# Kernel tuning notes

Measured on AMD Instinct MI355X. Metric: run time of the kernel, lower is better.

## Reference

```python
import jax, jax.numpy as jnp
import numpy as np
import math

T, B, C, H, W = 1, 64, 512, 8, 8
E, NH, MEM, FF = 512, 8, 32, 2048
HD = E // NH            # 64 per-head channels
TOT = HD * H * W        # 4096 = flattened per-head dim (channels x spatial)


def conv2d(x, w, b):
    # NCHW conv with 'same' padding, matching torch.nn.Conv2d(padding='same')
    y = jax.lax.conv_general_dilated(x, w, (1, 1), 'SAME',
                                     dimension_numbers=('NCHW', 'OIHW', 'NCHW'))
    return y + b[None, :, None, None]


def layernorm(x, w, b, eps=1e-5):
    # LayerNorm over (C,H,W) with elementwise affine, matching nn.LayerNorm((C,H,W))
    m = jnp.mean(x, axis=(1, 2, 3), keepdims=True)
    v = jnp.var(x, axis=(1, 2, 3), keepdims=True)
    return (x - m) * jax.lax.rsqrt(v + eps) * w[None] + b[None]


def setup_inputs() -> dict:
    key = jax.random.key(0)
    ks = jax.random.split(key, 16)
    s = 0.02
    inp = {
        'input': jax.random.normal(ks[0], (T, B, C, H, W), jnp.float32),
        'attn_mask': jax.random.randint(ks[1], (B * NH, T, MEM), 0, 2) == 1,
        'concat_k': jax.random.normal(ks[2], (B, MEM, NH, TOT), jnp.float32),
        'concat_v': jax.random.normal(ks[3], (B, MEM, NH, TOT), jnp.float32),
        'proj_w': jax.random.normal(ks[4], (3 * E, C, 3, 3), jnp.float32) * s,
        'proj_b': jnp.zeros((3 * E,), jnp.float32),
        'out_w': jax.random.normal(ks[5], (E, E, 3, 3), jnp.float32) * s,
        'out_b': jnp.zeros((E,), jnp.float32),
        'lin1_w': jax.random.normal(ks[6], (FF, E, 3, 3), jnp.float32) * s,
        'lin1_b': jnp.zeros((FF,), jnp.float32),
        'lin2_w': jax.random.normal(ks[7], (E, FF, 3, 3), jnp.float32) * s,
        'lin2_b': jnp.zeros((E,), jnp.float32),
        'n1_w': jnp.ones((E, H, W), jnp.float32),
        'n1_b': jnp.zeros((E, H, W), jnp.float32),
        'n2_w': jnp.ones((E, H, W), jnp.float32),
        'n2_b': jnp.zeros((E, H, W), jnp.float32),
        'pos_w': jax.random.normal(ks[8], (MEM, H * W * E), jnp.float32) * s,
        'pos_b': jax.random.uniform(ks[9], (MEM, NH), jnp.float32, -0.1, 0.1),
    }
    return inp


def reference(input, attn_mask, concat_k, concat_v, proj_w, proj_b, out_w, out_b,
              lin1_w, lin1_b, lin2_w, lin2_b, n1_w, n1_b, n2_w, n2_b, pos_w, pos_b):
    x = input.reshape(T * B, C, H, W)
    kqv = conv2d(x, proj_w, proj_b)                      # [B, 3E, H, W]
    k0, q0, v0 = kqv[:, :E], kqv[:, E:2 * E], kqv[:, 2 * E:]

    def split_heads(t):  # [T*B,E,H,W] -> [B*NH, T, TOT]
        return t.reshape(T, B * NH, HD, H, W).transpose(1, 0, 2, 3, 4).reshape(B * NH, T, TOT)

    k, q, v = split_heads(k0), split_heads(q0), split_heads(v0)
    q = q / math.sqrt(TOT)

    def mem_pre(c):  # [B,MEM,NH,TOT] -> [B*NH, MEM-1, TOT]
        return c[:, 1:].transpose(1, 0, 2, 3).reshape(MEM - 1, B * NH, TOT).transpose(1, 0, 2)

    k = jnp.concatenate([mem_pre(concat_k), k], axis=1)  # [B*NH, MEM, TOT]
    v = jnp.concatenate([mem_pre(concat_v), v], axis=1)

    # learned relative-position bias on keys and logits
    pw = jnp.broadcast_to(pos_w[:, None, :], (MEM, B, NH * TOT)).reshape(MEM, B * NH, TOT).transpose(1, 0, 2)
    pb = jnp.broadcast_to(pos_b[:, None, :], (MEM, B, NH)).reshape(MEM, B * NH).transpose(1, 0)
    k = k + pw

    mask = jnp.where(attn_mask, -jnp.inf, 0.0).astype(q.dtype)
    mask = mask.at[:, :, -1].set(5.0)                    # current step always attendable (+5 bias)
    logits = mask + jnp.einsum('bqd,bkd->bqk', q, k) + pb[:, None, :]
    w_attn = jax.nn.softmax(logits, axis=-1)             # [B*NH, T, MEM]
    attn = jnp.einsum('bqk,bkd->bqd', w_attn, v)         # [B*NH, T, TOT]
    attn = attn.transpose(1, 0, 2).reshape(B, E, H, W)

    out = conv2d(attn, out_w, out_b)
    ret_k = k.transpose(1, 0, 2).reshape(MEM, B, NH, TOT).transpose(1, 0, 2, 3)
    ret_v = v.transpose(1, 0, 2).reshape(MEM, B, NH, TOT).transpose(1, 0, 2, 3)

    # norm_first=False path
    out = out + x[:, :E]
    out = layernorm(out, n1_w, n1_b)
    ff = conv2d(jax.nn.relu(conv2d(out, lin1_w, lin1_b)), lin2_w, lin2_b)
    out = layernorm(out + ff, n2_w, n2_b)
    return (out[None], ret_k, ret_v)
```

## Files before the change

### kernel.cpp

```cpp
#include <hip/hip_runtime.h>
#include <hip/hip_bf16.h>
#include <stdint.h>

typedef __attribute__((ext_vector_type(8))) short bf16x8;
typedef __attribute__((ext_vector_type(4))) float f32x4;

static __device__ __forceinline__ unsigned short f2bf(float f) {
  union { float f; unsigned int u; } v; v.f = f;
  unsigned int u = v.u;
  return (unsigned short)((u + 0x7FFFu + ((u >> 16) & 1u)) >> 16);
}

static __device__ __forceinline__ void gld16(const void* g, void* l) {
  __builtin_amdgcn_global_load_lds(
      (const __attribute__((address_space(1))) unsigned int*)g,
      (__attribute__((address_space(3))) unsigned int*)l, 16, 0, 0);
}

__global__ __launch_bounds__(256) void k_zero(uint4* __restrict__ p, int n) {
  int i = blockIdx.x * 256 + threadIdx.x;
  if (i < n) p[i] = make_uint4(0u, 0u, 0u, 0u);
}

__global__ __launch_bounds__(256) void k_prep(
    const float* __restrict__ projw, const float* __restrict__ outw,
    const float* __restrict__ l1w, const float* __restrict__ l2w,
    const float* __restrict__ x,
    unsigned short* __restrict__ wbP, unsigned short* __restrict__ wbO,
    unsigned short* __restrict__ wbL1, unsigned short* __restrict__ wbL2,
    unsigned short* __restrict__ xp) {
  __shared__ float l[4608];
  int bid = blockIdx.x, t = threadIdx.x;
  if (bid < 6144) {
    const float* in; unsigned short* out; int o, C, c0;
    if (bid < 1536)      { in = projw; out = wbP;  o = bid;               C = 512;  c0 = 0; }
    else if (bid < 2048) { in = outw;  out = wbO;  o = bid - 1536;        C = 512;  c0 = 0; }
    else if (bid < 4096) { in = l1w;   out = wbL1; o = bid - 2048;        C = 512;  c0 = 0; }
    else                 { in = l2w;   out = wbL2; o = (bid - 4096) >> 2; C = 2048; c0 = ((bid - 4096) & 3) << 9; }
    const float* src = in + ((size_t)o * C + c0) * 9;
    for (int j = t; j < 4608; j += 256) l[j] = src[j];
    __syncthreads();
    unsigned short* dst = out + (size_t)o * 9 * C;
#pragma unroll
    for (int j = 0; j < 18; ++j) {
      int f = t * 18 + j;
      int tap = f >> 9, c = f & 511;
      dst[(size_t)tap * C + c0 + c] = f2bf(l[c * 9 + tap]);
    }
  } else {
    int idx = bid - 6144;
    int b = idx >> 3, c0 = (idx & 7) << 6;
    float (*lt)[65] = (float(*)[65])l;
    int cr = t >> 2, p0 = (t & 3) << 4;
    const float* src = x + ((size_t)b * 512 + c0 + cr) * 64 + p0;
#pragma unroll
    for (int j = 0; j < 4; ++j) {
      float4 v = *(const float4*)(src + j * 4);
      lt[cr][p0 + j * 4 + 0] = v.x; lt[cr][p0 + j * 4 + 1] = v.y;
      lt[cr][p0 + j * 4 + 2] = v.z; lt[cr][p0 + j * 4 + 3] = v.w;
    }
    __syncthreads();
    int pix = t >> 2, cc0 = (t & 3) << 4;
    size_t prow = (size_t)b * 100 + 11 + (pix >> 3) * 10 + (pix & 7);
    unsigned short pk[16];
#pragma unroll
    for (int j = 0; j < 16; ++j) pk[j] = f2bf(lt[cc0 + j][pix]);
    *(uint4*)(xp + prow * 512 + c0 + cc0) = *(const uint4*)pk;
    *(uint4*)(xp + prow * 512 + c0 + cc0 + 8) = *(const uint4*)(pk + 8);
  }
}

__global__ __launch_bounds__(256) void k_x2pad(const float* __restrict__ x,
                                               unsigned short* __restrict__ xp) {
  int b = blockIdx.x >> 3, c0 = (blockIdx.x & 7) << 6;
  int t = threadIdx.x;
  __shared__ float l[64][65];
  int cr = t >> 2, p0 = (t & 3) << 4;
  const float* src = x + ((size_t)b * 512 + c0 + cr) * 64 + p0;
#pragma unroll
  for (int j = 0; j < 4; ++j) {
    float4 v = *(const float4*)(src + j * 4);
    l[cr][p0 + j * 4 + 0] = v.x; l[cr][p0 + j * 4 + 1] = v.y;
    l[cr][p0 + j * 4 + 2] = v.z; l[cr][p0 + j * 4 + 3] = v.w;
  }
  __syncthreads();
  int pix = t >> 2, cc0 = (t & 3) << 4;
  size_t prow = (size_t)b * 100 + 11 + (pix >> 3) * 10 + (pix & 7);
  unsigned short pk[16];
#pragma unroll
  for (int j = 0; j < 16; ++j) pk[j] = f2bf(l[cc0 + j][pix]);
  *(uint4*)(xp + prow * 512 + c0 + cc0) = *(const uint4*)pk;
  *(uint4*)(xp + prow * 512 + c0 + cc0 + 8) = *(const uint4*)(pk + 8);
}

template <int EPI>
__global__ __launch_bounds__(256, 2) void k_gemm9(
    const unsigned short* __restrict__ Wt, int ldK,
    const unsigned short* __restrict__ Xp, int C, int tlog,
    int kiter, const float* __restrict__ bias,
    void* __restrict__ outv, int Cout, size_t zstride) {
  __shared__ unsigned short lds[2][2][8192];
  int t = threadIdx.x, lane = t & 63, wid = t >> 6;

  int gx = gridDim.x;
  int f = blockIdx.x + blockIdx.y * gx;
  int cpx = (gx * gridDim.y) >> 3;
  int fs = (f & 7) * cpx + (f >> 3);
  int bx = fs % gx, by = fs / gx;

  int O0 = bx << 7, M0 = by << 7;
  int kbase = blockIdx.z * kiter;
  int srow = lane >> 3, skg = (lane & 7) << 3;

  int wrow[4], pbv[4];
#pragma unroll
  for (int i = 0; i < 4; ++i) {
    int rl = wid * 8 + i * 32 + srow;
    wrow[i] = O0 + rl;
    int m = M0 + rl, b = m >> 6, pix = m & 63;
    pbv[i] = b * 100 + (pix >> 3) * 10 + (pix & 7);
  }

  f32x4 acc[4][4];
#pragma unroll
  for (int i = 0; i < 4; ++i)
#pragma unroll
    for (int j = 0; j < 4; ++j) acc[i][j] = (f32x4){0.f, 0.f, 0.f, 0.f};

  auto stage = [&](int buf, int kt) {
    int gk = kbase + kt;
    int tap = gk >> tlog;
    int c0 = (gk - (tap << tlog)) << 6;
    int toff = tap + 7 * ((tap * 11) >> 5);
#pragma unroll
    for (int i = 0; i < 4; ++i) {
      gld16(Wt + (size_t)wrow[i] * ldK + (gk << 6) + skg,
            &lds[buf][0][(wid * 8 + i * 32) * 64]);
      gld16(Xp + (size_t)(pbv[i] + toff) * C + c0 + skg,
            &lds[buf][1][(wid * 8 + i * 32) * 64]);
    }
  };

  int wr = wid >> 1, wc = wid & 1;
  int frow = lane & 15, fkb = (lane >> 4) << 3;

  auto compute = [&](int buf) {
    const unsigned short* Wl = &lds[buf][0][0];
    const unsigned short* Xl = &lds[buf][1][0];
#pragma unroll
    for (int kk = 0; kk < 2; ++kk) {
      bf16x8 af[4], bfv[4];
#pragma unroll
      for (int ff = 0; ff < 4; ++ff) {
        af[ff]  = *(const bf16x8*)(Wl + ((wr * 64 + ff * 16 + frow) << 6) + kk * 32 + fkb);
        bfv[ff] = *(const bf16x8*)(Xl + ((wc * 64 + ff * 16 + frow) << 6) + kk * 32 + fkb);
      }
#pragma unroll
      for (int fi = 0; fi < 4; ++fi)
#pragma unroll
        for (int fj = 0; fj < 4; ++fj)
          acc[fi][fj] = __builtin_amdgcn_mfma_f32_16x16x32_bf16(af[fi], bfv[fj], acc[fi][fj], 0, 0, 0);
    }
  };

  stage(0, 0);
  __syncthreads();
  for (int kt = 0; kt < kiter; ++kt) {
    int cur = kt & 1;
    if (kt + 1 < kiter) stage(cur ^ 1, kt + 1);
    compute(cur);
    __syncthreads();
  }

  int ob = O0 + wr * 64, mb = M0 + wc * 64;
  int r0 = (lane >> 4) << 2, cm = lane & 15;
  if (EPI == 4) {
    unsigned short* outp = (unsigned short*)outv;
#pragma unroll
    for (int fi = 0; fi < 4; ++fi) {
      int oo = ob + fi * 16 + r0;
      float4 bv = *(const float4*)(bias + oo);
#pragma unroll
      for (int fj = 0; fj < 4; ++fj) {
        int mm = mb + fj * 16 + cm;
        int bb = mm >> 6, pix = mm & 63;
        size_t prow = (size_t)bb * 100 + 11 + (pix >> 3) * 10 + (pix & 7);
        unsigned short pk[4];
        pk[0] = f2bf(fmaxf(acc[fi][fj][0] + bv.x, 0.f));
        pk[1] = f2bf(fmaxf(acc[fi][fj][1] + bv.y, 0.f));
        pk[2] = f2bf(fmaxf(acc[fi][fj][2] + bv.z, 0.f));
        pk[3] = f2bf(fmaxf(acc[fi][fj][3] + bv.w, 0.f));
        *(ushort4*)(outp + prow * Cout + oo) = *(const ushort4*)pk;
      }
    }
  } else {
    float* out = (float*)outv + (size_t)blockIdx.z * zstride;
#pragma unroll
    for (int fi = 0; fi < 4; ++fi) {
#pragma unroll
      for (int fj = 0; fj < 4; ++fj) {
        int mm = mb + fj * 16 + cm;
        int bb = mm >> 6, pix = mm & 63;
#pragma unroll
        for (int r = 0; r < 4; ++r) {
          int oo = ob + fi * 16 + r0 + r;
          float v = acc[fi][fj][r];
          if (EPI == 0) v += bias[oo];
          out[((size_t)bb * Cout + oo) * 64 + pix] = v;
        }
      }
    }
  }
}

__global__ __launch_bounds__(256) void k_sum2(const float* __restrict__ a,
                                              const float* __restrict__ b,
                                              const float* __restrict__ bias,
                                              float* __restrict__ o) {
  int i = (blockIdx.x * 256 + threadIdx.x) * 4;
  int ch = (i >> 6) % 1536;
  float4 va = *(const float4*)(a + i);
  float4 vb = *(const float4*)(b + i);
  float bs = bias[ch];
  *(float4*)(o + i) = make_float4(va.x + vb.x + bs, va.y + vb.y + bs,
                                  va.z + vb.z + bs, va.w + vb.w + bs);
}

__global__ __launch_bounds__(256) void k_attnK(
    const float* __restrict__ kqv, const float* __restrict__ ck,
    const float* __restrict__ pw, const float* __restrict__ pb,
    float* __restrict__ rk, float* __restrict__ logits) {
  int idx = blockIdx.x;
  int h = idx & 7, m = (idx >> 3) & 31, b = idx >> 8;
  int t = threadIdx.x, lane = t & 63, wid = t >> 6;
  int i0 = t << 4;
  int hd = i0 >> 6, pix = i0 & 63;

  const float* src = (m < 31)
      ? (ck + (((size_t)(b * 32 + m + 1) * 8 + h) << 12) + i0)
      : (kqv + ((size_t)(b * 1536 + h * 64 + hd) << 6) + pix);
  const float* qs = kqv + ((size_t)(b * 1536 + 512 + h * 64 + hd) << 6) + pix;
  const float* pws = pw + ((size_t)m << 15) + (h << 12) + i0;
  float* dst = rk + (((size_t)(b * 32 + m) * 8 + h) << 12) + i0;

  float part = 0.f;
#pragma unroll
  for (int j = 0; j < 4; ++j) {
    float4 a = *(const float4*)(src + j * 4);
    float4 p = *(const float4*)(pws + j * 4);
    float4 q = *(const float4*)(qs + j * 4);
    float4 kk;
    kk.x = a.x + p.x; kk.y = a.y + p.y; kk.z = a.z + p.z; kk.w = a.w + p.w;
    *(float4*)(dst + j * 4) = kk;
    part += 0.015625f * (q.x * kk.x + q.y * kk.y + q.z * kk.z + q.w * kk.w);
  }
#pragma unroll
  for (int s = 32; s; s >>= 1) part += __shfl_xor(part, s);
  __shared__ float red[4];
  if (lane == 0) red[wid] = part;
  __syncthreads();
  if (t == 0)
    logits[((b << 3) + h) * 32 + m] = red[0] + red[1] + red[2] + red[3] + pb[m * 8 + h];
}

__global__ __launch_bounds__(256) void k_attnV(
    const float* __restrict__ kqv, const int* __restrict__ mask,
    const float* __restrict__ cv, const float* __restrict__ logits,
    float* __restrict__ rv, float* __restrict__ attnb) {
  int bh = blockIdx.x, b = bh >> 3, h = bh & 7;
  int t = threadIdx.x;
  int d = (blockIdx.y << 10) + (t << 2);
  int hd = d >> 6, pix = d & 63;

  float lg[32];
#pragma unroll
  for (int j = 0; j < 8; ++j) {
    float4 v = *(const float4*)(logits + bh * 32 + j * 4);
    lg[j * 4 + 0] = v.x; lg[j * 4 + 1] = v.y; lg[j * 4 + 2] = v.z; lg[j * 4 + 3] = v.w;
  }
  float mx = -INFINITY;
#pragma unroll
  for (int m = 0; m < 32; ++m) {
    if (m == 31) lg[m] += 5.0f;
    else if (mask[bh * 32 + m] != 0) lg[m] = -INFINITY;
    mx = fmaxf(mx, lg[m]);
  }
  float sm = 0.f;
#pragma unroll
  for (int m = 0; m < 32; ++m) { lg[m] = __expf(lg[m] - mx); sm += lg[m]; }
  float rs = 1.f / sm;

  float4 acc = make_float4(0.f, 0.f, 0.f, 0.f);
  for (int m = 0; m < 32; ++m) {
    const float* src = (m < 31)
        ? (cv + (((size_t)(b * 32 + m + 1) * 8 + h) << 12) + d)
        : (kqv + ((size_t)(b * 1536 + 1024 + h * 64 + hd) << 6) + pix);
    float4 v = *(const float4*)src;
    *(float4*)(rv + (((size_t)(b * 32 + m) * 8 + h) << 12) + d) = v;
    float wm = lg[m] * rs;
    acc.x += wm * v.x; acc.y += wm * v.y; acc.z += wm * v.z; acc.w += wm * v.w;
  }
  *(float4*)(attnb + ((size_t)(b * 512 + h * 64 + hd) << 6) + pix) = acc;
}

__global__ __launch_bounds__(256) void k_lnstat(
    const float* __restrict__ p, const float* __restrict__ resid,
    const float* __restrict__ bias, float* __restrict__ xbuf,
    float2* __restrict__ stat) {
  int bb = blockIdx.x, seg = blockIdx.y, t = threadIdx.x;
  int lane = t & 63, wid = t >> 6;
  size_t base = (size_t)bb << 15;
  float s = 0.f, sq = 0.f;
#pragma unroll
  for (int j = 0; j < 4; ++j) {
    int i = (seg << 12) + t * 4 + j * 1024;
    float4 v0 = *(const float4*)(p + base + i);
    float4 v1 = *(const float4*)(p + 2097152 + base + i);
    float4 v2 = *(const float4*)(p + 4194304 + base + i);
    float4 v3 = *(const float4*)(p + 6291456 + base + i);
    float4 vr = *(const float4*)(resid + base + i);
    float bs = bias[i >> 6];
    float4 xx;
    xx.x = v0.x + v1.x + v2.x + v3.x + vr.x + bs;
    xx.y = v0.y + v1.y + v2.y + v3.y + vr.y + bs;
    xx.z = v0.z + v1.z + v2.z + v3.z + vr.z + bs;
    xx.w = v0.w + v1.w + v2.w + v3.w + vr.w + bs;
    *(float4*)(xbuf + base + i) = xx;
    s += xx.x + xx.y + xx.z + xx.w;
    sq += xx.x * xx.x + xx.y * xx.y + xx.z * xx.z + xx.w * xx.w;
  }
#pragma unroll
  for (int k = 32; k; k >>= 1) { s += __shfl_xor(s, k); sq += __shfl_xor(sq, k); }
  __shared__ float rsm[4], rqm[4];
  if (lane == 0) { rsm[wid] = s; rqm[wid] = sq; }
  __syncthreads();
  if (t == 0)
    stat[bb * 8 + seg] = make_float2(rsm[0] + rsm[1] + rsm[2] + rsm[3],
                                     rqm[0] + rqm[1] + rqm[2] + rqm[3]);
}

__global__ __launch_bounds__(256) void k_lnapply(
    const float* __restrict__ xbuf, const float2* __restrict__ stat,
    const float* __restrict__ w, const float* __restrict__ beta,
    float* __restrict__ out) {
  int bb = blockIdx.x, seg = blockIdx.y, t = threadIdx.x;
  size_t base = (size_t)bb << 15;
  float s = 0.f, sq = 0.f;
#pragma unroll
  for (int k = 0; k < 8; ++k) {
    float2 st = stat[bb * 8 + k];
    s += st.x; sq += st.y;
  }
  float mean = s * (1.f / 32768.f);
  float var = sq * (1.f / 32768.f) - mean * mean;
  float rinv = rsqrtf(var + 1e-5f);
#pragma unroll
  for (int j = 0; j < 4; ++j) {
    int i = (seg << 12) + t * 4 + j * 1024;
    float4 xx = *(const float4*)(xbuf + base + i);
    float4 vw = *(const float4*)(w + i);
    float4 vt = *(const float4*)(beta + i);
    float4 r;
    r.x = (xx.x - mean) * rinv * vw.x + vt.x;
    r.y = (xx.y - mean) * rinv * vw.y + vt.y;
    r.z = (xx.z - mean) * rinv * vw.z + vt.z;
    r.w = (xx.w - mean) * rinv * vw.w + vt.w;
    *(float4*)(out + base + i) = r;
  }
}

extern "C" void kernel_launch(void* const* d_in, const int* in_sizes, int n_in,
                              void* d_out, int out_size, void* d_ws, size_t ws_size,
                              hipStream_t stream) {
  const float* x     = (const float*)d_in[0];
  const int*   mask  = (const int*)d_in[1];
  const float* ck    = (const float*)d_in[2];
  const float* cv    = (const float*)d_in[3];
  const float* projw = (const float*)d_in[4];
  const float* projb = (const float*)d_in[5];
  const float* outw  = (const float*)d_in[6];
  const float* outb  = (const float*)d_in[7];
  const float* l1w   = (const float*)d_in[8];
  const float* l1b   = (const float*)d_in[9];
  const float* l2w   = (const float*)d_in[10];
  const float* l2b   = (const float*)d_in[11];
  const float* n1w   = (const float*)d_in[12];
  const float* n1b   = (const float*)d_in[13];
  const float* n2w   = (const float*)d_in[14];
  const float* n2b   = (const float*)d_in[15];
  const float* posw  = (const float*)d_in[16];
  const float* posb  = (const float*)d_in[17];

  char* ws = (char*)d_ws;
  unsigned short* wbP   = (unsigned short*)(ws);
  unsigned short* wbO   = (unsigned short*)(ws + 14155776);
  unsigned short* wbL1  = (unsigned short*)(ws + 18874368);
  unsigned short* wbL2  = (unsigned short*)(ws + 37748736);
  unsigned short* xpadI = (unsigned short*)(ws + 56623104);
  unsigned short* apad  = (unsigned short*)(ws + 63176704);
  unsigned short* l1pad = (unsigned short*)(ws + 69730304);
  unsigned short* ffpad = (unsigned short*)(ws + 76283904);
  float* kqvA   = (float*)(ws + 102498304);
  float* kqvB   = (float*)(ws + 127664128);
  float* kqv    = (float*)(ws + 152829952);
  float* logits = (float*)(ws + 177995776);
  float* res    = (float*)(ws + 178061312);
  float* ln1    = (float*)(ws + 211615744);
  float* attnb  = (float*)(ws + 220004352);
  float* xbuf1  = (float*)(ws + 228392960);
  float* xbuf2  = (float*)(ws + 236781568);
  float2* stat1 = (float2*)(ws + 245170176);
  float2* stat2 = (float2*)(ws + 245174272);

  float* out0 = (float*)d_out;
  float* rk = out0 + 2097152;
  float* rv = rk + 67108864;

  k_zero<<<11200, 256, 0, stream>>>((uint4*)(ws + 56623104), 2867200);

  k_prep<<<6656, 256, 0, stream>>>(projw, outw, l1w, l2w, x, wbP, wbO, wbL1, wbL2, xpadI);

  k_gemm9<3><<<dim3(12, 32, 2), 256, 0, stream>>>(wbP, 4608, xpadI, 512, 3, 36, nullptr, kqvA, 1536, 6291456);
  k_sum2<<<6144, 256, 0, stream>>>(kqvA, kqvB, projb, kqv);

  k_attnK<<<16384, 256, 0, stream>>>(kqv, ck, posw, posb, rk, logits);
  k_attnV<<<dim3(512, 4), 256, 0, stream>>>(kqv, mask, cv, logits, rv, attnb);
  k_x2pad<<<512, 256, 0, stream>>>(attnb, apad);

  k_gemm9<3><<<dim3(4, 32, 4), 256, 0, stream>>>(wbO, 4608, apad, 512, 3, 18, nullptr, res, 512, 2097152);
  k_lnstat<<<dim3(64, 8), 256, 0, stream>>>(res, x, outb, xbuf1, stat1);
  k_lnapply<<<dim3(64, 8), 256, 0, stream>>>(xbuf1, stat1, n1w, n1b, ln1);
  k_x2pad<<<512, 256, 0, stream>>>(ln1, l1pad);

  k_gemm9<4><<<dim3(16, 32, 1), 256, 0, stream>>>(wbL1, 4608, l1pad, 512, 3, 72, l1b, ffpad, 2048, 0);

  k_gemm9<3><<<dim3(4, 32, 4), 256, 0, stream>>>(wbL2, 18432, ffpad, 2048, 5, 72, nullptr, res, 512, 2097152);
  k_lnstat<<<dim3(64, 8), 256, 0, stream>>>(res, ln1, l2b, xbuf2, stat2);
  k_lnapply<<<dim3(64, 8), 256, 0, stream>>>(xbuf2, stat2, n2w, n2b, out0);
}
```

Baseline: 750.3 us.

## Fuse split-K sum into attention, zero only pad borders, fuse LN1 with pad

Drops the separate k_sum2 pass: the attention K and V kernels now read both split-K partial buffers and add the projection bias inline. The full-buffer zeroing kernel is replaced by zeroing only the 36 border rows per image inside k_prep. LayerNorm-1 apply and the bf16 padded transpose are merged into one kernel. This saves several launches and full-tensor round trips, but the query partials are now re-read once per memory slot in k_attnK.

New measurement: 769.6 us. +2.6%, slower.

```diff
diff --git a/kernel.cpp b/kernel.cpp
--- a/kernel.cpp
+++ b/kernel.cpp
@@ -15,11 +15,6 @@
   __builtin_amdgcn_global_load_lds(
       (const __attribute__((address_space(1))) unsigned int*)g,
       (__attribute__((address_space(3))) unsigned int*)l, 16, 0, 0);
-}
-
-__global__ __launch_bounds__(256) void k_zero(uint4* __restrict__ p, int n) {
-  int i = blockIdx.x * 256 + threadIdx.x;
-  if (i < n) p[i] = make_uint4(0u, 0u, 0u, 0u);
 }
 
 __global__ __launch_bounds__(256) void k_prep(
@@ -28,15 +23,35 @@
     const float* __restrict__ x,
     unsigned short* __restrict__ wbP, unsigned short* __restrict__ wbO,
     unsigned short* __restrict__ wbL1, unsigned short* __restrict__ wbL2,
-    unsigned short* __restrict__ xp) {
+    unsigned short* __restrict__ xp, unsigned short* __restrict__ apad,
+    unsigned short* __restrict__ l1pad, unsigned short* __restrict__ ffpad) {
+  int bid = blockIdx.x, t = threadIdx.x;
+  if (bid < 9216) {
+    int buf = bid / 2304, rem = bid - buf * 2304;
+    int b = rem / 36, ridx = rem - b * 36;
+    int row;
+    if (ridx < 11) row = ridx;
+    else if (ridx < 25) { int p = ridx - 11; row = 19 + (p >> 1) * 10 + (p & 1); }
+    else row = 89 + (ridx - 25);
+    unsigned short* ptr; int C;
+    switch (buf) {
+      case 0: ptr = xp;    C = 512;  break;
+      case 1: ptr = apad;  C = 512;  break;
+      case 2: ptr = l1pad; C = 512;  break;
+      default: ptr = ffpad; C = 2048; break;
+    }
+    int n16 = C >> 3;
+    if (t < n16) *(uint4*)(ptr + ((size_t)b * 100 + row) * C + t * 8) = make_uint4(0u, 0u, 0u, 0u);
+    return;
+  }
   __shared__ float l[4608];
-  int bid = blockIdx.x, t = threadIdx.x;
-  if (bid < 6144) {
+  int id = bid - 9216;
+  if (id < 6144) {
     const float* in; unsigned short* out; int o, C, c0;
-    if (bid < 1536)      { in = projw; out = wbP;  o = bid;               C = 512;  c0 = 0; }
-    else if (bid < 2048) { in = outw;  out = wbO;  o = bid - 1536;        C = 512;  c0 = 0; }
-    else if (bid < 4096) { in = l1w;   out = wbL1; o = bid - 2048;        C = 512;  c0 = 0; }
-    else                 { in = l2w;   out = wbL2; o = (bid - 4096) >> 2; C = 2048; c0 = ((bid - 4096) & 3) << 9; }
+    if (id < 1536)      { in = projw; out = wbP;  o = id;               C = 512;  c0 = 0; }
+    else if (id < 2048) { in = outw;  out = wbO;  o = id - 1536;        C = 512;  c0 = 0; }
+    else if (id < 4096) { in = l1w;   out = wbL1; o = id - 2048;        C = 512;  c0 = 0; }
+    else                { in = l2w;   out = wbL2; o = (id - 4096) >> 2; C = 2048; c0 = ((id - 4096) & 3) << 9; }
     const float* src = in + ((size_t)o * C + c0) * 9;
     for (int j = t; j < 4608; j += 256) l[j] = src[j];
     __syncthreads();
@@ -48,7 +63,7 @@
       dst[(size_t)tap * C + c0 + c] = f2bf(l[c * 9 + tap]);
     }
   } else {
-    int idx = bid - 6144;
+    int idx = id - 6144;
     int b = idx >> 3, c0 = (idx & 7) << 6;
     float (*lt)[65] = (float(*)[65])l;
     int cr = t >> 2, p0 = (t & 3) << 4;
@@ -213,21 +228,9 @@
   }
 }
 
-__global__ __launch_bounds__(256) void k_sum2(const float* __restrict__ a,
-                                              const float* __restrict__ b,
-                                              const float* __restrict__ bias,
-                                              float* __restrict__ o) {
-  int i = (blockIdx.x * 256 + threadIdx.x) * 4;
-  int ch = (i >> 6) % 1536;
-  float4 va = *(const float4*)(a + i);
-  float4 vb = *(const float4*)(b + i);
-  float bs = bias[ch];
-  *(float4*)(o + i) = make_float4(va.x + vb.x + bs, va.y + vb.y + bs,
-                                  va.z + vb.z + bs, va.w + vb.w + bs);
-}
-
 __global__ __launch_bounds__(256) void k_attnK(
-    const float* __restrict__ kqv, const float* __restrict__ ck,
+    const float* __restrict__ kqvA, const float* __restrict__ kqvB,
+    const float* __restrict__ projb, const float* __restrict__ ck,
     const float* __restrict__ pw, const float* __restrict__ pb,
     float* __restrict__ rk, float* __restrict__ logits) {
   int idx = blockIdx.x;
@@ -236,23 +239,43 @@
   int i0 = t << 4;
   int hd = i0 >> 6, pix = i0 & 63;
 
-  const float* src = (m < 31)
-      ? (ck + (((size_t)(b * 32 + m + 1) * 8 + h) << 12) + i0)
-      : (kqv + ((size_t)(b * 1536 + h * 64 + hd) << 6) + pix);
-  const float* qs = kqv + ((size_t)(b * 1536 + 512 + h * 64 + hd) << 6) + pix;
+  size_t qoff = ((size_t)(b * 1536 + 512 + h * 64 + hd) << 6) + pix;
   const float* pws = pw + ((size_t)m << 15) + (h << 12) + i0;
   float* dst = rk + (((size_t)(b * 32 + m) * 8 + h) << 12) + i0;
+  float bq = projb[512 + h * 64 + hd];
 
   float part = 0.f;
-#pragma unroll
-  for (int j = 0; j < 4; ++j) {
-    float4 a = *(const float4*)(src + j * 4);
-    float4 p = *(const float4*)(pws + j * 4);
-    float4 q = *(const float4*)(qs + j * 4);
-    float4 kk;
-    kk.x = a.x + p.x; kk.y = a.y + p.y; kk.z = a.z + p.z; kk.w = a.w + p.w;
-    *(float4*)(dst + j * 4) = kk;
-    part += 0.015625f * (q.x * kk.x + q.y * kk.y + q.z * kk.z + q.w * kk.w);
+  if (m < 31) {
+    const float* src = ck + (((size_t)(b * 32 + m + 1) * 8 + h) << 12) + i0;
+#pragma unroll
+    for (int j = 0; j < 4; ++j) {
+      float4 a = *(const float4*)(src + j * 4);
+      float4 p = *(const float4*)(pws + j * 4);
+      float4 qa = *(const float4*)(kqvA + qoff + j * 4);
+      float4 qb = *(const float4*)(kqvB + qoff + j * 4);
+      float4 kk;
+      kk.x = a.x + p.x; kk.y = a.y + p.y; kk.z = a.z + p.z; kk.w = a.w + p.w;
+      *(float4*)(dst + j * 4) = kk;
+      part += 0.015625f * ((qa.x + qb.x + bq) * kk.x + (qa.y + qb.y + bq) * kk.y +
+                           (qa.z + qb.z + bq) * kk.z + (qa.w + qb.w + bq) * kk.w);
+    }
+  } else {
+    size_t koff = ((size_t)(b * 1536 + h * 64 + hd) << 6) + pix;
+    float bk = projb[h * 64 + hd];
+#pragma unroll
+    for (int j = 0; j < 4; ++j) {
+      float4 ka = *(const float4*)(kqvA + koff + j * 4);
+      float4 kb = *(const float4*)(kqvB + koff + j * 4);
+      float4 p = *(const float4*)(pws + j * 4);
+      float4 qa = *(const float4*)(kqvA + qoff + j * 4);
+      float4 qb = *(const float4*)(kqvB + qoff + j * 4);
+      float4 kk;
+      kk.x = ka.x + kb.x + bk + p.x; kk.y = ka.y + kb.y + bk + p.y;
+      kk.z = ka.z + kb.z + bk + p.z; kk.w = ka.w + kb.w + bk + p.w;
+      *(float4*)(dst + j * 4) = kk;
+      part += 0.015625f * ((qa.x + qb.x + bq) * kk.x + (qa.y + qb.y + bq) * kk.y +
+                           (qa.z + qb.z + bq) * kk.z + (qa.w + qb.w + bq) * kk.w);
+    }
   }
 #pragma unroll
   for (int s = 32; s; s >>= 1) part += __shfl_xor(part, s);
@@ -264,7 +287,8 @@
 }
 
 __global__ __launch_bounds__(256) void k_attnV(
-    const float* __restrict__ kqv, const int* __restrict__ mask,
+    const float* __restrict__ kqvA, const float* __restrict__ kqvB,
+    const float* __restrict__ projb, const int* __restrict__ mask,
     const float* __restrict__ cv, const float* __restrict__ logits,
     float* __restrict__ rv, float* __restrict__ attnb) {
   int bh = blockIdx.x, b = bh >> 3, h = bh & 7;
@@ -291,13 +315,23 @@
   float rs = 1.f / sm;
 
   float4 acc = make_float4(0.f, 0.f, 0.f, 0.f);
-  for (int m = 0; m < 32; ++m) {
-    const float* src = (m < 31)
-        ? (cv + (((size_t)(b * 32 + m + 1) * 8 + h) << 12) + d)
-        : (kqv + ((size_t)(b * 1536 + 1024 + h * 64 + hd) << 6) + pix);
+  for (int m = 0; m < 31; ++m) {
+    const float* src = cv + (((size_t)(b * 32 + m + 1) * 8 + h) << 12) + d;
     float4 v = *(const float4*)src;
     *(float4*)(rv + (((size_t)(b * 32 + m) * 8 + h) << 12) + d) = v;
     float wm = lg[m] * rs;
+    acc.x += wm * v.x; acc.y += wm * v.y; acc.z += wm * v.z; acc.w += wm * v.w;
+  }
+  {
+    size_t voff = ((size_t)(b * 1536 + 1024 + h * 64 + hd) << 6) + pix;
+    float bv = projb[1024 + h * 64 + hd];
+    float4 va = *(const float4*)(kqvA + voff);
+    float4 vb = *(const float4*)(kqvB + voff);
+    float4 v;
+    v.x = va.x + vb.x + bv; v.y = va.y + vb.y + bv;
+    v.z = va.z + vb.z + bv; v.w = va.w + vb.w + bv;
+    *(float4*)(rv + (((size_t)(b * 32 + 31) * 8 + h) << 12) + d) = v;
+    float wm = lg[31] * rs;
     acc.x += wm * v.x; acc.y += wm * v.y; acc.z += wm * v.z; acc.w += wm * v.w;
   }
   *(float4*)(attnb + ((size_t)(b * 512 + h * 64 + hd) << 6) + pix) = acc;
@@ -367,6 +401,50 @@
     r.w = (xx.w - mean) * rinv * vw.w + vt.w;
     *(float4*)(out + base + i) = r;
   }
+}
+
+__global__ __launch_bounds__(256) void k_lnpad(
+    const float* __restrict__ xbuf, const float2* __restrict__ stat,
+    const float* __restrict__ w, const float* __restrict__ beta,
+    float* __restrict__ ln1, unsigned short* __restrict__ lp) {
+  int b = blockIdx.x >> 3, c0 = (blockIdx.x & 7) << 6;
+  int t = threadIdx.x;
+  float s = 0.f, sq = 0.f;
+#pragma unroll
+  for (int k = 0; k < 8; ++k) {
+    float2 st = stat[b * 8 + k];
+    s += st.x; sq += st.y;
+  }
+  float mean = s * (1.f / 32768.f);
+  float var = sq * (1.f / 32768.f) - mean * mean;
+  float rinv = rsqrtf(var + 1e-5f);
+
+  __shared__ float l[64][65];
+  int cr = t >> 2, p0 = (t & 3) << 4;
+  size_t off = ((size_t)b * 512 + c0 + cr) * 64 + p0;
+  size_t woff = ((size_t)(c0 + cr)) * 64 + p0;
+#pragma unroll
+  for (int j = 0; j < 4; ++j) {
+    float4 xx = *(const float4*)(xbuf + off + j * 4);
+    float4 vw = *(const float4*)(w + woff + j * 4);
+    float4 vt = *(const float4*)(beta + woff + j * 4);
+    float4 r;
+    r.x = (xx.x - mean) * rinv * vw.x + vt.x;
+    r.y = (xx.y - mean) * rinv * vw.y + vt.y;
+    r.z = (xx.z - mean) * rinv * vw.z + vt.z;
+    r.w = (xx.w - mean) * rinv * vw.w + vt.w;
+    *(float4*)(ln1 + off + j * 4) = r;
+    l[cr][p0 + j * 4 + 0] = r.x; l[cr][p0 + j * 4 + 1] = r.y;
+    l[cr][p0 + j * 4 + 2] = r.z; l[cr][p0 + j * 4 + 3] = r.w;
+  }
+  __syncthreads();
+  int pix = t >> 2, cc0 = (t & 3) << 4;
+  size_t prow = (size_t)b * 100 + 11 + (pix >> 3) * 10 + (pix & 7);
+  unsigned short pk[16];
+#pragma unroll
+  for (int j = 0; j < 16; ++j) pk[j] = f2bf(l[cc0 + j][pix]);
+  *(uint4*)(lp + prow * 512 + c0 + cc0) = *(const uint4*)pk;
+  *(uint4*)(lp + prow * 512 + c0 + cc0 + 8) = *(const uint4*)(pk + 8);
 }
 
 extern "C" void kernel_launch(void* const* d_in, const int* in_sizes, int n_in,
@@ -402,7 +480,6 @@
   unsigned short* ffpad = (unsigned short*)(ws + 76283904);
   float* kqvA   = (float*)(ws + 102498304);
   float* kqvB   = (float*)(ws + 127664128);
-  float* kqv    = (float*)(ws + 152829952);
   float* logits = (float*)(ws + 177995776);
   float* res    = (float*)(ws + 178061312);
   float* ln1    = (float*)(ws + 211615744);
@@ -416,21 +493,18 @@
   float* rk = out0 + 2097152;
   float* rv = rk + 67108864;
 
-  k_zero<<<11200, 256, 0, stream>>>((uint4*)(ws + 56623104), 2867200);
-
-  k_prep<<<6656, 256, 0, stream>>>(projw, outw, l1w, l2w, x, wbP, wbO, wbL1, wbL2, xpadI);
+  k_prep<<<15872, 256, 0, stream>>>(projw, outw, l1w, l2w, x,
+                                    wbP, wbO, wbL1, wbL2, xpadI, apad, l1pad, ffpad);
 
   k_gemm9<3><<<dim3(12, 32, 2), 256, 0, stream>>>(wbP, 4608, xpadI, 512, 3, 36, nullptr, kqvA, 1536, 6291456);
-  k_sum2<<<6144, 256, 0, stream>>>(kqvA, kqvB, projb, kqv);
-
-  k_attnK<<<16384, 256, 0, stream>>>(kqv, ck, posw, posb, rk, logits);
-  k_attnV<<<dim3(512, 4), 256, 0, stream>>>(kqv, mask, cv, logits, rv, attnb);
+
+  k_attnK<<<16384, 256, 0, stream>>>(kqvA, kqvB, projb, ck, posw, posb, rk, logits);
+  k_attnV<<<dim3(512, 4), 256, 0, stream>>>(kqvA, kqvB, projb, mask, cv, logits, rv, attnb);
   k_x2pad<<<512, 256, 0, stream>>>(attnb, apad);
 
   k_gemm9<3><<<dim3(4, 32, 4), 256, 0, stream>>>(wbO, 4608, apad, 512, 3, 18, nullptr, res, 512, 2097152);
   k_lnstat<<<dim3(64, 8), 256, 0, stream>>>(res, x, outb, xbuf1, stat1);
-  k_lnapply<<<dim3(64, 8), 256, 0, stream>>>(xbuf1, stat1, n1w, n1b, ln1);
-  k_x2pad<<<512, 256, 0, stream>>>(ln1, l1pad);
+  k_lnpad<<<512, 256, 0, stream>>>(xbuf1, stat1, n1w, n1b, ln1, l1pad);
 
   k_gemm9<4><<<dim3(16, 32, 1), 256, 0, stream>>>(wbL1, 4608, l1pad, 512, 3, 72, l1b, ffpad, 2048, 0);
 
```
